# Kernel tuning notes

Measured on AMD Instinct MI355X. Metric: run time of the kernel, lower is better.

The kernel has to match this reference:

```python
import jax, jax.numpy as jnp
import numpy as np

B, DIM, HEADS, H, W = 8, 384, 8, 128, 128
EPS = 1e-12  # torch F.normalize eps


def _conv1x1(x, w):
    # x: [b,c,h,w], w: [out,in] -> [b,out,h,w]
    return jnp.einsum('oc,bchw->bohw', w, x)


def _dwconv3x3(x, w):
    # depthwise 3x3, groups=DIM; w: [DIM,1,3,3]
    return jax.lax.conv_general_dilated(
        x, w, window_strides=(1, 1), padding='SAME',
        feature_group_count=DIM,
        dimension_numbers=('NCHW', 'OIHW', 'NCHW'))


def _l2norm(t):
    # F.normalize along last dim
    n = jnp.sqrt(jnp.sum(t * t, axis=-1, keepdims=True))
    return t / jnp.maximum(n, EPS)


def setup_inputs() -> dict:
    key = jax.random.key(0)
    ks = jax.random.split(key, 9)
    s = 0.02
    return {
        'x': jax.random.normal(ks[0], (B, DIM, H, W), jnp.float32),
        'w0': jax.random.normal(ks[1], (DIM, DIM), jnp.float32) * s,
        'w1': jax.random.normal(ks[2], (DIM, DIM), jnp.float32) * s,
        'w2': jax.random.normal(ks[3], (DIM, DIM), jnp.float32) * s,
        'dw0': jax.random.normal(ks[4], (DIM, 1, 3, 3), jnp.float32) * s,
        'dw1': jax.random.normal(ks[5], (DIM, 1, 3, 3), jnp.float32) * s,
        'dw2': jax.random.normal(ks[6], (DIM, 1, 3, 3), jnp.float32) * s,
        'wproj': jax.random.normal(ks[7], (DIM, DIM), jnp.float32) * s,
        'temp': jnp.ones((HEADS, 1, 1), jnp.float32),
    }


def reference(x, w0, w1, w2, dw0, dw1, dw2, wproj, temp):
    b, c, h, w = x.shape
    ch = c // HEADS
    q = _dwconv3x3(_conv1x1(x, w0), dw0)
    k = _dwconv3x3(_conv1x1(x, w1), dw1)
    v = _dwconv3x3(_conv1x1(x, w2), dw2)
    # b (head c) h w -> b head c (h w)
    q = _l2norm(q.reshape(b, HEADS, ch, h * w))
    k = _l2norm(k.reshape(b, HEADS, ch, h * w))
    v = v.reshape(b, HEADS, ch, h * w)
    attn = jax.nn.softmax(jnp.einsum('bhcn,bhdn->bhcd', q, k) * temp, axis=-1)
    out = jnp.einsum('bhcd,bhdn->bhcn', attn, v).reshape(b, c, h, w)
    return _conv1x1(out, wproj)
```

## Files before the change

### kernel.cpp

```cpp
#include <hip/hip_runtime.h>
#include <math.h>

#define DIMC 384
#define NHEADS 8
#define CHD 48
#define HWN 16384
#define IMW 128
#define PERT ((size_t)DIMC * HWN)
#define WELEM (DIMC * DIMC)
#define NB 8

typedef short short8 __attribute__((ext_vector_type(8)));
typedef unsigned short u16x8 __attribute__((ext_vector_type(8)));
typedef float f32x4 __attribute__((ext_vector_type(4)));

__device__ __forceinline__ unsigned short f2bf(float f) {
  unsigned int u = __float_as_uint(f);
  unsigned int r = (u + 0x7fffu + ((u >> 16) & 1u)) >> 16;
  return (unsigned short)r;
}
__device__ __forceinline__ float bf2f(unsigned short b) {
  return __uint_as_float(((unsigned int)b) << 16);
}
__device__ __forceinline__ void async16(const void* g, void* l) {
  __builtin_amdgcn_global_load_lds(
      (const __attribute__((address_space(1))) void*)g,
      (__attribute__((address_space(3))) void*)l, 16, 0, 0);
}

template <int OUTBF>
__device__ __forceinline__ void gemm384_body(
    const unsigned short* __restrict__ A,
    const unsigned short* __restrict__ BT,
    void* __restrict__ Y, int nbase)
{
  __shared__ unsigned short As[2][24576];
  __shared__ unsigned short Bs[2][8192];
  const int tid = threadIdx.x;
  const int lane = tid & 63;
  const int wv = tid >> 6;
  const int wm = (wv >> 1) * 96;
  const int wn = (wv & 1) * 64;

  f32x4 acc[6][4];
#pragma unroll
  for (int i = 0; i < 6; ++i)
#pragma unroll
    for (int j = 0; j < 4; ++j) acc[i][j] = (f32x4){0.f, 0.f, 0.f, 0.f};

  const unsigned short* asrc = A + (size_t)(tid >> 3) * DIMC + (tid & 7) * 8;
  const unsigned short* bsrc =
      BT + (size_t)(nbase + (tid >> 3)) * DIMC + (tid & 7) * 8;

  const int ar = wm + (lane & 15);
  const int br = wn + (lane & 15);
  const int kg = (lane >> 4) << 4;
  const int sw = (lane & 7) << 4;

#define WAITVM(n) asm volatile("s_waitcnt vmcnt(" #n ")" ::: "memory")
#define SBAR()                                 \
  do {                                         \
    __builtin_amdgcn_sched_barrier(0);         \
    __builtin_amdgcn_s_barrier();              \
    __builtin_amdgcn_sched_barrier(0);         \
  } while (0)

#define STAGE(buf, k0)                                                   \
  do {                                                                   \
    _Pragma("unroll") for (int i = 0; i < 6; ++i)                        \
        async16(asrc + (size_t)(i * 64) * DIMC + (k0),                   \
                &As[buf][(size_t)(tid + i * 512) * 8]);                  \
    _Pragma("unroll") for (int i = 0; i < 2; ++i)                        \
        async16(bsrc + (size_t)(i * 64) * DIMC + (k0),                   \
                &Bs[buf][(size_t)(tid + i * 512) * 8]);                  \
  } while (0)

#define COMPUTE(buf)                                                     \
  do {                                                                   \
    short8 af[2][6], bf[2][4];                                           \
    _Pragma("unroll") for (int kq = 0; kq < 2; ++kq) {                   \
      const int kb = kq * 64 + kg;                                       \
      _Pragma("unroll") for (int mi = 0; mi < 6; ++mi)                   \
          af[kq][mi] = *reinterpret_cast<const short8*>(                 \
              (const char*)&As[buf][0] + (ar + mi * 16) * 128 + (kb ^ sw)); \
      _Pragma("unroll") for (int ni = 0; ni < 4; ++ni)                   \
          bf[kq][ni] = *reinterpret_cast<const short8*>(                 \
              (const char*)&Bs[buf][0] + (br + ni * 16) * 128 + (kb ^ sw)); \
    }                                                                    \
    __builtin_amdgcn_s_setprio(1);                                       \
    _Pragma("unroll") for (int kq = 0; kq < 2; ++kq)                     \
      _Pragma("unroll") for (int mi = 0; mi < 6; ++mi)                   \
        _Pragma("unroll") for (int ni = 0; ni < 4; ++ni)                 \
          acc[mi][ni] = __builtin_amdgcn_mfma_f32_16x16x32_bf16(         \
              af[kq][mi], bf[kq][ni], acc[mi][ni], 0, 0, 0);             \
    __builtin_amdgcn_s_setprio(0);                                       \
  } while (0)

  STAGE(0, 0);
  WAITVM(0); SBAR();
  STAGE(1, 64);            COMPUTE(0);
  SBAR(); STAGE(0, 128); WAITVM(8); SBAR(); COMPUTE(1);
  SBAR(); STAGE(1, 192); WAITVM(8); SBAR(); COMPUTE(0);
  SBAR(); STAGE(0, 256); WAITVM(8); SBAR(); COMPUTE(1);
  SBAR(); STAGE(1, 320); WAITVM(8); SBAR(); COMPUTE(0);
  WAITVM(0); SBAR(); COMPUTE(1);

#undef STAGE
#undef COMPUTE
#undef WAITVM
#undef SBAR

  const int orow = wm + ((lane >> 4) << 2);
  const int ocol = nbase + wn + (lane & 15);
#pragma unroll
  for (int mi = 0; mi < 6; ++mi)
#pragma unroll
    for (int ni = 0; ni < 4; ++ni)
#pragma unroll
      for (int r = 0; r < 4; ++r) {
        size_t off = (size_t)(orow + mi * 16 + r) * HWN + ocol + ni * 16;
        if (OUTBF) ((unsigned short*)Y)[off] = f2bf(acc[mi][ni][r]);
        else       ((float*)Y)[off] = acc[mi][ni][r];
      }
}

__global__ __launch_bounds__(512) void k_conv_mfma(
    const unsigned short* __restrict__ Wc, const unsigned short* __restrict__ XT,
    unsigned short* __restrict__ Y)
{
  int g0 = (int)blockIdx.y * 128 + blockIdx.x;
  int lin = g0 * 3 + blockIdx.z;
  int swz = (lin & 7) * 384 + (lin >> 3);
  int g = swz / 3, j = swz - g * 3;
  int bb = g >> 7, nt = g & 127;
  gemm384_body<1>(Wc + j * WELEM, XT + (size_t)bb * PERT,
                  Y + (size_t)bb * 3 * PERT + (size_t)j * PERT, nt * 128);
}

__global__ __launch_bounds__(512) void k_final_mfma(
    const unsigned short* __restrict__ M, const unsigned short* __restrict__ vT,
    float* __restrict__ out)
{
  int lin = (int)blockIdx.y * 128 + blockIdx.x;
  int swz = (lin & 7) * 128 + (lin >> 3);
  int bb = swz >> 7, nt = swz & 127;
  gemm384_body<0>(M + (size_t)bb * WELEM, vT + (size_t)bb * PERT,
                  out + (size_t)bb * PERT, nt * 128);
}

__global__ __launch_bounds__(256) void k_transpose_x(
    const float* __restrict__ x, unsigned short* __restrict__ XT)
{
  __shared__ unsigned short S[64][72];
  int n0 = blockIdx.x * 64, c0 = blockIdx.y * 64;
  const float* xb = x + (size_t)blockIdx.z * PERT;
  unsigned short* XTb = XT + (size_t)blockIdx.z * PERT;
  int t = threadIdx.x;
  int cl = t >> 2, ns = (t & 3) * 16;
  const float* src = &xb[(size_t)(c0 + cl) * HWN + n0 + ns];
#pragma unroll
  for (int i = 0; i < 16; i += 4) {
    float4 v = *reinterpret_cast<const float4*>(&src[i]);
    S[cl][ns + i + 0] = f2bf(v.x);
    S[cl][ns + i + 1] = f2bf(v.y);
    S[cl][ns + i + 2] = f2bf(v.z);
    S[cl][ns + i + 3] = f2bf(v.w);
  }
  __syncthreads();
  int nl = t >> 2, cs = (t & 3) * 16;
  unsigned short tmp[16];
#pragma unroll
  for (int i = 0; i < 16; ++i) tmp[i] = S[cs + i][nl];
  u16x8 p0, p1;
#pragma unroll
  for (int i = 0; i < 8; ++i) { p0[i] = tmp[i]; p1[i] = tmp[8 + i]; }
  char* rowb = (char*)XTb + (size_t)(n0 + nl) * (DIMC * 2);
  int cb = (c0 + cs) * 2;
  int sw = (nl & 7) << 4;
  *reinterpret_cast<u16x8*>(rowb + ((cb) ^ sw)) = p0;
  *reinterpret_cast<u16x8*>(rowb + ((cb + 16) ^ sw)) = p1;
}

__global__ __launch_bounds__(256) void k_convert_w(
    const float* __restrict__ w0, const float* __restrict__ w1,
    const float* __restrict__ w2, unsigned short* __restrict__ Wc)
{
  int idx = blockIdx.x * 256 + threadIdx.x;
  int j = idx / WELEM, r = idx - j * WELEM;
  int m = r / DIMC, k = r - m * DIMC;
  const float* s = (j == 0) ? w0 : (j == 1) ? w1 : w2;
  int kd = (k & ~63) | ((k & 63) ^ ((m & 7) << 3));
  Wc[j * WELEM + m * DIMC + kd] = f2bf(s[r]);
}

__global__ __launch_bounds__(256) void k_dwconv(
    const unsigned short* __restrict__ Yin, const float* __restrict__ dw0,
    const float* __restrict__ dw1,
    unsigned short* __restrict__ Zout, float* __restrict__ partial)
{
  __shared__ float red[4];
  int gid = blockIdx.x * 256 + threadIdx.x;
  int plane = gid >> 10;
  int rem = gid & 1023;
  int b = plane / 768;
  int pl = plane - b * 768;
  int j = pl / DIMC;
  int c = pl - j * DIMC;
  int h = rem >> 3;
  int wg = (rem & 7) << 4;
  int lane = threadIdx.x & 63;
  const float* dw = ((j == 0) ? dw0 : dw1) + c * 9;
  const unsigned short* src = Yin + ((size_t)(b * 3 + j) * DIMC + c) * HWN;

  float acc[16];
#pragma unroll
  for (int i = 0; i < 16; ++i) acc[i] = 0.f;

#pragma unroll
  for (int dy = -1; dy <= 1; ++dy) {
    int hh = h + dy;
    bool valid = (hh >= 0) && (hh < IMW);
    float mf[16];
    if (valid) {
      const unsigned short* row = src + hh * IMW + wg;
      u16x8 a0 = *reinterpret_cast<const u16x8*>(row);
      u16x8 a1 = *reinterpret_cast<const u16x8*>(row + 8);
#pragma unroll
      for (int i = 0; i < 8; ++i) { mf[i] = bf2f(a0[i]); mf[8 + i] = bf2f(a1[i]); }
    } else {
#pragma unroll
      for (int i = 0; i < 16; ++i) mf[i] = 0.f;
    }
    float lf = __shfl_up(mf[15], 1);
    float rf = __shfl_down(mf[0], 1);
    if ((lane & 7) == 0) lf = 0.f;
    if ((lane & 7) == 7) rf = 0.f;
    float t0 = dw[(dy + 1) * 3], t1 = dw[(dy + 1) * 3 + 1], t2 = dw[(dy + 1) * 3 + 2];
    acc[0] = fmaf(lf, t0, fmaf(mf[0], t1, fmaf(mf[1], t2, acc[0])));
#pragma unroll
    for (int i = 1; i < 15; ++i)
      acc[i] = fmaf(mf[i - 1], t0, fmaf(mf[i], t1, fmaf(mf[i + 1], t2, acc[i])));
    acc[15] = fmaf(mf[14], t0, fmaf(mf[15], t1, fmaf(rf, t2, acc[15])));
  }

  u16x8 o0, o1;
#pragma unroll
  for (int i = 0; i < 8; ++i) { o0[i] = f2bf(acc[i]); o1[i] = f2bf(acc[8 + i]); }
  unsigned short* dst =
      Zout + ((size_t)(b * 3 + j) * DIMC + c) * HWN + h * IMW + wg;
  *reinterpret_cast<u16x8*>(dst) = o0;
  *reinterpret_cast<u16x8*>(dst + 8) = o1;

  float s = 0.f;
#pragma unroll
  for (int i = 0; i < 16; ++i) s = fmaf(acc[i], acc[i], s);
#pragma unroll
  for (int off = 32; off > 0; off >>= 1) s += __shfl_down(s, off);
  if ((threadIdx.x & 63) == 0) red[threadIdx.x >> 6] = s;
  __syncthreads();
  if (threadIdx.x == 0)
    partial[blockIdx.x] = red[0] + red[1] + red[2] + red[3];
}

__global__ __launch_bounds__(256) void k_dwconv_v(
    const unsigned short* __restrict__ Yin, const float* __restrict__ dw2,
    unsigned short* __restrict__ vT)
{
  __shared__ unsigned short S[128][40];
  int h = blockIdx.x;
  int cgrp = blockIdx.y;
  int b = blockIdx.z;
  int t = threadIdx.x;
  int c_l = t >> 3;
  int seg = t & 7;
  int wg = seg << 4;
  int lane = t & 63;
  int c = cgrp * 32 + c_l;
  const float* dw = dw2 + c * 9;
  const unsigned short* src = Yin + ((size_t)(b * 3 + 2) * DIMC + c) * HWN;

  float acc[16];
#pragma unroll
  for (int i = 0; i < 16; ++i) acc[i] = 0.f;

#pragma unroll
  for (int dy = -1; dy <= 1; ++dy) {
    int hh = h + dy;
    bool valid = (hh >= 0) && (hh < IMW);
    float mf[16];
    if (valid) {
      const unsigned short* row = src + hh * IMW + wg;
      u16x8 a0 = *reinterpret_cast<const u16x8*>(row);
      u16x8 a1 = *reinterpret_cast<const u16x8*>(row + 8);
#pragma unroll
      for (int i = 0; i < 8; ++i) { mf[i] = bf2f(a0[i]); mf[8 + i] = bf2f(a1[i]); }
    } else {
#pragma unroll
      for (int i = 0; i < 16; ++i) mf[i] = 0.f;
    }
    float lf = __shfl_up(mf[15], 1);
    float rf = __shfl_down(mf[0], 1);
    if ((lane & 7) == 0) lf = 0.f;
    if ((lane & 7) == 7) rf = 0.f;
    float t0 = dw[(dy + 1) * 3], t1 = dw[(dy + 1) * 3 + 1], t2 = dw[(dy + 1) * 3 + 2];
    acc[0] = fmaf(lf, t0, fmaf(mf[0], t1, fmaf(mf[1], t2, acc[0])));
#pragma unroll
    for (int i = 1; i < 15; ++i)
      acc[i] = fmaf(mf[i - 1], t0, fmaf(mf[i], t1, fmaf(mf[i + 1], t2, acc[i])));
    acc[15] = fmaf(mf[14], t0, fmaf(mf[15], t1, fmaf(rf, t2, acc[15])));
  }

#pragma unroll
  for (int i = 0; i < 16; ++i) S[wg + i][c_l] = f2bf(acc[i]);
  __syncthreads();

  int px = t >> 1, half = t & 1;
  int n = h * IMW + px;
  u16x8 p0 = *reinterpret_cast<const u16x8*>(&S[px][half * 16]);
  u16x8 p1 = *reinterpret_cast<const u16x8*>(&S[px][half * 16 + 8]);
  char* rowb = (char*)(vT + (size_t)b * PERT) + (size_t)n * (DIMC * 2);
  int cb = (cgrp * 32 + half * 16) * 2;
  int sw = (n & 7) << 4;
  int chunk = cb & ~127, off = cb & 127;
  *reinterpret_cast<u16x8*>(rowb + chunk + ((off) ^ sw)) = p0;
  *reinterpret_cast<u16x8*>(rowb + chunk + ((off + 16) ^ sw)) = p1;
}

__global__ __launch_bounds__(256) void k_qk_mfma(
    const unsigned short* __restrict__ qkv, float* __restrict__ Spart)
{
  __shared__ float Sred[4][2304];
  int blk = blockIdx.x;
  int b = blk >> 6, h = (blk >> 3) & 7, slice = blk & 7;
  int tid = threadIdx.x, lane = tid & 63, w = tid >> 6;
  const unsigned short* qb = qkv + ((size_t)b * 3 * DIMC + h * CHD) * HWN;
  const unsigned short* kb = qb + (size_t)DIMC * HWN;
  const int row = lane & 15;
  const int ko = (lane >> 4) << 3;
  const int n0 = slice * 2048 + w * 512;

  f32x4 acc[3][3];
#pragma unroll
  for (int i = 0; i < 3; ++i)
#pragma unroll
    for (int j = 0; j < 3; ++j) acc[i][j] = (f32x4){0.f, 0.f, 0.f, 0.f};

  for (int ns = n0; ns < n0 + 512; ns += 32) {
    short8 aq[3], bk[3];
#pragma unroll
    for (int mi = 0; mi < 3; ++mi)
      aq[mi] = *reinterpret_cast<const short8*>(&qb[(size_t)(mi * 16 + row) * HWN + ns + ko]);
#pragma unroll
    for (int ni = 0; ni < 3; ++ni)
      bk[ni] = *reinterpret_cast<const short8*>(&kb[(size_t)(ni * 16 + row) * HWN + ns + ko]);
#pragma unroll
    for (int mi = 0; mi < 3; ++mi)
#pragma unroll
      for (int ni = 0; ni < 3; ++ni)
        acc[mi][ni] = __builtin_amdgcn_mfma_f32_16x16x32_bf16(
            aq[mi], bk[ni], acc[mi][ni], 0, 0, 0);
  }
  const int c0 = (lane >> 4) << 2;
#pragma unroll
  for (int mi = 0; mi < 3; ++mi)
#pragma unroll
    for (int ni = 0; ni < 3; ++ni)
#pragma unroll
      for (int r = 0; r < 4; ++r)
        Sred[w][(mi * 16 + c0 + r) * 48 + ni * 16 + row] = acc[mi][ni][r];
  __syncthreads();
  float* dst = Spart + (size_t)blk * 2304;
#pragma unroll
  for (int i = 0; i < 9; ++i) {
    int e = tid + i * 256;
    dst[e] = Sred[0][e] + Sred[1][e] + Sred[2][e] + Sred[3][e];
  }
}

__global__ __launch_bounds__(384) void k_attn_sm(
    const float* __restrict__ Spart, const float* __restrict__ partial,
    const float* __restrict__ temp, float* __restrict__ Aat)
{
  __shared__ float sk[DIMC];
  int b = blockIdx.x, t = threadIdx.x;
  int h = t / CHD, c = t - h * CHD;
  float sq = 0.f, skk = 0.f;
#pragma unroll
  for (int s = 0; s < 4; ++s) {
    sq  += partial[((size_t)b * 768 + t) * 4 + s];
    skk += partial[((size_t)b * 768 + DIMC + t) * 4 + s];
  }
  sk[t] = 1.f / fmaxf(sqrtf(skk), 1e-12f);
  float invq = 1.f / fmaxf(sqrtf(sq), 1e-12f);
  __syncthreads();
  float vals[CHD];
#pragma unroll
  for (int d = 0; d < CHD; ++d) vals[d] = 0.f;
  for (int sl = 0; sl < 8; ++sl) {
    const float* sp = Spart + (size_t)(b * 64 + h * 8 + sl) * 2304 + c * 48;
#pragma unroll
    for (int d = 0; d < CHD; ++d) vals[d] += sp[d];
  }
  float tp = temp[h];
  float vq = invq * tp;
  float mx = -1e30f;
#pragma unroll
  for (int d = 0; d < CHD; ++d) {
    vals[d] *= vq * sk[h * CHD + d];
    mx = fmaxf(mx, vals[d]);
  }
  float sum = 0.f;
#pragma unroll
  for (int d = 0; d < CHD; ++d) { vals[d] = expf(vals[d] - mx); sum += vals[d]; }
  float inv = 1.f / sum;
  float* Arow = Aat + ((size_t)(b * 8 + h) * 48 + c) * 48;
#pragma unroll
  for (int d = 0; d < CHD; ++d) Arow[d] = vals[d] * inv;
}

__global__ __launch_bounds__(256) void k_combine(
    const float* __restrict__ wproj, const float* __restrict__ Aat,
    unsigned short* __restrict__ M)
{
  int idx = blockIdx.x * 256 + threadIdx.x;
  int b = idx / WELEM;
  int r2 = idx - b * WELEM;
  int o = r2 / DIMC;
  int dg = r2 - o * DIMC;
  int h = dg / CHD, d = dg - h * CHD;
  const float* wrow = wproj + (size_t)o * DIMC + h * CHD;
  const float* Acol = Aat + (size_t)b * DIMC * CHD + (size_t)(h * CHD) * CHD + d;
  float s = 0.f;
#pragma unroll
  for (int c = 0; c < CHD; ++c)
    s = fmaf(wrow[c], Acol[c * CHD], s);
  int dd = (dg & ~63) | ((dg & 63) ^ ((o & 7) << 3));
  M[b * WELEM + o * DIMC + dd] = f2bf(s);
}

extern "C" void kernel_launch(void* const* d_in, const int* in_sizes, int n_in,
                              void* d_out, int out_size, void* d_ws, size_t ws_size,
                              hipStream_t stream)
{
  const float* x     = (const float*)d_in[0];
  const float* w0    = (const float*)d_in[1];
  const float* w1    = (const float*)d_in[2];
  const float* w2    = (const float*)d_in[3];
  const float* dw0   = (const float*)d_in[4];
  const float* dw1   = (const float*)d_in[5];
  const float* dw2   = (const float*)d_in[6];
  const float* wproj = (const float*)d_in[7];
  const float* temp  = (const float*)d_in[8];
  float* out = (float*)d_out;

  char* p = (char*)d_ws;
  unsigned short* Wc     = (unsigned short*)p;  p += (size_t)3 * WELEM * 2;
  unsigned short* XT     = (unsigned short*)p;  p += (size_t)NB * PERT * 2;
  unsigned short* q0k0v0 = (unsigned short*)p;  p += (size_t)NB * 3 * PERT * 2;
  unsigned short* qkv    = (unsigned short*)p;  p += (size_t)NB * 3 * PERT * 2;
  float* Spart   = (float*)p;  p += (size_t)512 * 2304 * 4;
  float* Aat     = (float*)p;  p += (size_t)NB * DIMC * CHD * 4;
  float* partial = (float*)p;  p += (size_t)NB * 2 * DIMC * 4 * 4;
  unsigned short* Mbf = (unsigned short*)p;
  unsigned short* vT = XT;

  k_convert_w<<<(3 * WELEM + 255) / 256, 256, 0, stream>>>(w0, w1, w2, Wc);
  k_transpose_x<<<dim3(256, 6, NB), 256, 0, stream>>>(x, XT);
  k_conv_mfma<<<dim3(128, NB, 3), 512, 0, stream>>>(Wc, XT, q0k0v0);
  k_dwconv<<<NB * 2 * DIMC * 4, 256, 0, stream>>>(q0k0v0, dw0, dw1, qkv, partial);
  k_dwconv_v<<<dim3(128, 12, NB), 256, 0, stream>>>(q0k0v0, dw2, vT);
  k_qk_mfma<<<512, 256, 0, stream>>>(qkv, Spart);
  k_attn_sm<<<NB, 384, 0, stream>>>(Spart, partial, temp, Aat);
  k_combine<<<(NB * WELEM) / 256, 256, 0, stream>>>(wproj, Aat, Mbf);
  k_final_mfma<<<dim3(128, NB), 512, 0, stream>>>(Mbf, vT, out);
  (void)in_sizes; (void)n_in; (void)out_size; (void)ws_size;
}
```

Before: 557.8 us.

## Restructure qkv 1x1 conv GEMM to keep weight tile resident across N tiles

The qkv projection GEMM now uses 256-thread blocks that each load a 128x384 weight slice into LDS once, then loop over four 128-column N tiles, streaming only the activation tiles with double buffering. Previously every 384x128 output tile reloaded the full 384x384 weight. The aim is to cut redundant weight traffic and LDS staging per output. In exchange each block carries a longer serial loop and a smaller per-block tile (128x128 instead of 384x128), so activation columns are reread for each of the three M tiles, and the grid has 2304 blocks.

```diff
diff --git a/kernel.cpp b/kernel.cpp
--- a/kernel.cpp
+++ b/kernel.cpp
@@ -28,6 +28,126 @@
       (__attribute__((address_space(3))) void*)l, 16, 0, 0);
 }
 
+#define WAITVM(n) asm volatile("s_waitcnt vmcnt(" #n ")" ::: "memory")
+#define SBAR()                                 \
+  do {                                         \
+    __builtin_amdgcn_sched_barrier(0);         \
+    __builtin_amdgcn_s_barrier();              \
+    __builtin_amdgcn_sched_barrier(0);         \
+  } while (0)
+
+__global__ __launch_bounds__(256) void k_conv_mfma(
+    const unsigned short* __restrict__ Wc, const unsigned short* __restrict__ XT,
+    unsigned short* __restrict__ Y)
+{
+  __shared__ unsigned short Ap[6][8192];
+  __shared__ unsigned short Bs[2][8192];
+
+  int lin = (int)blockIdx.x;
+  int swz = (lin & 7) * 288 + (lin >> 3);
+  int g = swz / 9, r = swz - g * 9;
+  int b = g >> 5, nc = g & 31;
+  int j = r / 3, mt = r - j * 3;
+
+  const unsigned short* A = Wc + j * WELEM + (size_t)(mt * 128) * DIMC;
+  const unsigned short* XTb = XT + (size_t)b * PERT;
+  unsigned short* Yb = Y + (size_t)b * 3 * PERT + (size_t)j * PERT;
+  const int nbase0 = nc * 512;
+
+  const int tid = threadIdx.x;
+  const int lane = tid & 63;
+  const int wv = tid >> 6;
+  const int wm = (wv >> 1) * 64;
+  const int wn = (wv & 1) * 64;
+
+  const unsigned short* asrc = A + (size_t)(tid >> 3) * DIMC + (tid & 7) * 8;
+  const unsigned short* bsrc =
+      XTb + (size_t)(nbase0 + (tid >> 3)) * DIMC + (tid & 7) * 8;
+
+  const int ar = wm + (lane & 15);
+  const int br = wn + (lane & 15);
+  const int kg = (lane >> 4) << 4;
+  const int sw = (lane & 7) << 4;
+
+  f32x4 acc[4][4];
+#pragma unroll
+  for (int i = 0; i < 4; ++i)
+#pragma unroll
+    for (int jj = 0; jj < 4; ++jj) acc[i][jj] = (f32x4){0.f, 0.f, 0.f, 0.f};
+
+#define STAGE_B(buf, nt, t)                                              \
+  do {                                                                   \
+    _Pragma("unroll") for (int i = 0; i < 4; ++i)                        \
+        async16(bsrc + (size_t)((nt) * 128 + i * 32) * DIMC + (t) * 64,  \
+                &Bs[buf][(size_t)(tid + i * 256) * 8]);                  \
+  } while (0)
+
+#define COMPUTE(kc, buf)                                                 \
+  do {                                                                   \
+    short8 af[2][4], bf[2][4];                                           \
+    _Pragma("unroll") for (int kq = 0; kq < 2; ++kq) {                   \
+      const int kb = kq * 64 + kg;                                       \
+      _Pragma("unroll") for (int mi = 0; mi < 4; ++mi)                   \
+          af[kq][mi] = *reinterpret_cast<const short8*>(                 \
+              (const char*)&Ap[kc][0] + (ar + mi * 16) * 128 + (kb ^ sw)); \
+      _Pragma("unroll") for (int ni = 0; ni < 4; ++ni)                   \
+          bf[kq][ni] = *reinterpret_cast<const short8*>(                 \
+              (const char*)&Bs[buf][0] + (br + ni * 16) * 128 + (kb ^ sw)); \
+    }                                                                    \
+    __builtin_amdgcn_s_setprio(1);                                       \
+    _Pragma("unroll") for (int kq = 0; kq < 2; ++kq)                     \
+      _Pragma("unroll") for (int mi = 0; mi < 4; ++mi)                   \
+        _Pragma("unroll") for (int ni = 0; ni < 4; ++ni)                 \
+          acc[mi][ni] = __builtin_amdgcn_mfma_f32_16x16x32_bf16(         \
+              af[kq][mi], bf[kq][ni], acc[mi][ni], 0, 0, 0);             \
+    __builtin_amdgcn_s_setprio(0);                                       \
+  } while (0)
+
+#pragma unroll
+  for (int kc = 0; kc < 6; ++kc)
+#pragma unroll
+    for (int i = 0; i < 4; ++i)
+      async16(asrc + (size_t)(i * 32) * DIMC + kc * 64,
+              &Ap[kc][(size_t)(tid + i * 256) * 8]);
+  STAGE_B(0, 0, 0);
+
+  for (int nt = 0; nt < 4; ++nt) {
+#pragma unroll
+    for (int t = 0; t < 6; ++t) {
+      const int buf = t & 1;
+      SBAR();
+      if (t < 5) {
+        STAGE_B(buf ^ 1, nt, t + 1);
+        WAITVM(4); SBAR();
+      } else if (nt < 3) {
+        STAGE_B(0, nt + 1, 0);
+        WAITVM(4); SBAR();
+      } else {
+        WAITVM(0); SBAR();
+      }
+      COMPUTE(t, buf);
+    }
+    {
+      const int orow = mt * 128 + wm + ((lane >> 4) << 2);
+      const int ocol = nbase0 + nt * 128 + wn + (lane & 15);
+#pragma unroll
+      for (int mi = 0; mi < 4; ++mi)
+#pragma unroll
+        for (int ni = 0; ni < 4; ++ni)
+#pragma unroll
+          for (int rr = 0; rr < 4; ++rr)
+            Yb[(size_t)(orow + mi * 16 + rr) * HWN + ocol + ni * 16] =
+                f2bf(acc[mi][ni][rr]);
+#pragma unroll
+      for (int i = 0; i < 4; ++i)
+#pragma unroll
+        for (int jj = 0; jj < 4; ++jj) acc[i][jj] = (f32x4){0.f, 0.f, 0.f, 0.f};
+    }
+  }
+#undef STAGE_B
+#undef COMPUTE
+}
+
 template <int OUTBF>
 __device__ __forceinline__ void gemm384_body(
     const unsigned short* __restrict__ A,
@@ -56,14 +176,6 @@
   const int br = wn + (lane & 15);
   const int kg = (lane >> 4) << 4;
   const int sw = (lane & 7) << 4;
-
-#define WAITVM(n) asm volatile("s_waitcnt vmcnt(" #n ")" ::: "memory")
-#define SBAR()                                 \
-  do {                                         \
-    __builtin_amdgcn_sched_barrier(0);         \
-    __builtin_amdgcn_s_barrier();              \
-    __builtin_amdgcn_sched_barrier(0);         \
-  } while (0)
 
 #define STAGE(buf, k0)                                                   \
   do {                                                                   \
@@ -107,8 +219,6 @@
 
 #undef STAGE
 #undef COMPUTE
-#undef WAITVM
-#undef SBAR
 
   const int orow = wm + ((lane >> 4) << 2);
   const int ocol = nbase + wn + (lane & 15);
@@ -122,19 +232,6 @@
         if (OUTBF) ((unsigned short*)Y)[off] = f2bf(acc[mi][ni][r]);
         else       ((float*)Y)[off] = acc[mi][ni][r];
       }
-}
-
-__global__ __launch_bounds__(512) void k_conv_mfma(
-    const unsigned short* __restrict__ Wc, const unsigned short* __restrict__ XT,
-    unsigned short* __restrict__ Y)
-{
-  int g0 = (int)blockIdx.y * 128 + blockIdx.x;
-  int lin = g0 * 3 + blockIdx.z;
-  int swz = (lin & 7) * 384 + (lin >> 3);
-  int g = swz / 3, j = swz - g * 3;
-  int bb = g >> 7, nt = g & 127;
-  gemm384_body<1>(Wc + j * WELEM, XT + (size_t)bb * PERT,
-                  Y + (size_t)bb * 3 * PERT + (size_t)j * PERT, nt * 128);
 }
 
 __global__ __launch_bounds__(512) void k_final_mfma(
@@ -466,7 +563,7 @@
 
   k_convert_w<<<(3 * WELEM + 255) / 256, 256, 0, stream>>>(w0, w1, w2, Wc);
   k_transpose_x<<<dim3(256, 6, NB), 256, 0, stream>>>(x, XT);
-  k_conv_mfma<<<dim3(128, NB, 3), 512, 0, stream>>>(Wc, XT, q0k0v0);
+  k_conv_mfma<<<2304, 256, 0, stream>>>(Wc, XT, q0k0v0);
   k_dwconv<<<NB * 2 * DIMC * 4, 256, 0, stream>>>(q0k0v0, dw0, dw1, qkv, partial);
   k_dwconv_v<<<dim3(128, 12, NB), 256, 0, stream>>>(q0k0v0, dw2, vT);
   k_qk_mfma<<<512, 256, 0, stream>>>(qkv, Spart);
```

After: 648.4 us. 1.16x slower.
